# Kernel tuning notes

Hardware: AMD Instinct MI355X
Metric: run time of the kernel (lower is better)

Reference implementation:

```python
import jax, jax.numpy as jnp
import numpy as np

BUFFER_SIZE = 64  # chunk size == sliding window size


def setup_inputs() -> dict:
    key = jax.random.key(0)
    k1, k2, k3, k4 = jax.random.split(key, 4)
    B, S, dim = 4, 8192, 256
    D = dim * 2
    states = jax.random.normal(k1, (B, S, dim, 2), dtype=jnp.float32)
    # projection weights (module inits them to identity; use scaled random for a
    # non-trivial but numerically tame reference)
    Wq = jax.random.normal(k2, (D, D), dtype=jnp.float32) * 0.05
    Wk = jax.random.normal(k3, (D, D), dtype=jnp.float32) * 0.05
    Wv = jax.random.normal(k4, (D, D), dtype=jnp.float32) * 0.05
    return {"states": states, "Wq": Wq, "Wk": Wk, "Wv": Wv}


def reference(states, Wq, Wk, Wv):
    B, S, dim, _ = states.shape
    D = dim * 2
    C = BUFFER_SIZE
    assert S % C == 0 and S > 2 * C
    n = S // C  # number of chunks

    x = states.reshape(B, S, D)
    q = x @ Wq.T
    k = x @ Wk.T
    v = x @ Wv.T

    # chunk: [B, n, C, D]
    qc = q.reshape(B, n, C, D)
    kc = k.reshape(B, n, C, D)
    vc = v.reshape(B, n, C, D)

    # context for chunk i = chunk i-1 ++ chunk i  -> [B, n, 2C, D]
    zeros_blk = jnp.zeros_like(kc[:, :1])
    k_ctx = jnp.concatenate([jnp.concatenate([zeros_blk, kc[:, :-1]], axis=1), kc], axis=2)
    v_ctx = jnp.concatenate([jnp.concatenate([zeros_blk, vc[:, :-1]], axis=1), vc], axis=2)

    scale = 1.0 / jnp.sqrt(jnp.asarray(D, dtype=q.dtype))
    scores = jnp.einsum('bnqd,bnkd->bnqk', qc, k_ctx) * scale  # [B, n, C, 2C]

    # mask: query at local pos qi attends keys strictly before it (global),
    # i.e. context index j < C + qi; chunk 0 has no previous chunk (j >= C).
    qi = jnp.arange(C)[:, None]            # [C,1]
    j = jnp.arange(2 * C)[None, :]         # [1,2C]
    chunk_idx = jnp.arange(n)[:, None, None]
    mask = (j < C + qi)[None] & ((chunk_idx > 0) | (j >= C)[None])  # [n, C, 2C]

    scores = jnp.where(mask[None], scores, jnp.asarray(-1e30, scores.dtype))
    p = jax.nn.softmax(scores, axis=-1)
    # fully-masked rows (only global position 0) -> zero output
    row_valid = jnp.any(mask, axis=-1, keepdims=True)[None].astype(p.dtype)
    p = p * row_valid

    out = jnp.einsum('bnqk,bnkd->bnqd', p, v_ctx).reshape(B, S, D)
    out = out.at[:, 0, :].set(0.0)  # matches retrieved_flat[:, 0, :] = 0.0
    return out.reshape(B, S, dim, 2)
```

## Files before the change

kernel.cpp:

```cpp
#include <hip/hip_runtime.h>

#define SCALE 0.044194173824159216f

typedef _Float16 half8 __attribute__((ext_vector_type(8)));
typedef _Float16 half4 __attribute__((ext_vector_type(4)));
typedef float    f32x4 __attribute__((ext_vector_type(4)));

#define MFMA(A, B, Cc) __builtin_amdgcn_mfma_f32_16x16x32_f16((A), (B), (Cc), 0, 0, 0)

#define X16_OFF 0ull
#define Y16_OFF 33554432ull
#define MT_OFF  67108864ull
#define MP_OFF  68157440ull
#define VT_OFF  100663296ull
#define W16_OFF 134217728ull
#define WS_NEED 135790592ull

typedef __attribute__((address_space(1))) const unsigned int glb_t;
typedef __attribute__((address_space(3))) unsigned int lds_t;

__device__ __forceinline__ void gl16(const void* g, void* l) {
  __builtin_amdgcn_global_load_lds((glb_t*)g, (lds_t*)l, 16, 0, 0);
}

__device__ __forceinline__ half8 ldf64(const _Float16* buf, int row, int colh) {
  int byte = row * 128 + (((colh) << 1) ^ ((row & 7) << 4));
  return *(const half8*)((const char*)buf + byte);
}
__device__ __forceinline__ half8 ldf128(const _Float16* buf, int row, int colh) {
  int byte = row * 256 + (((colh) << 1) ^ ((row & 7) << 4));
  return *(const half8*)((const char*)buf + byte);
}

__global__ __launch_bounds__(256)
void k0_cvt(const float* __restrict__ x, const float* __restrict__ Wq,
            const float* __restrict__ Wk, const float* __restrict__ Wv,
            _Float16* __restrict__ x16, _Float16* __restrict__ w16)
{
  const long long NX = 16777216LL;
  long long base = ((long long)blockIdx.x * 256 + threadIdx.x) * 8;
  const float* src;
  _Float16* dst;
  float sc = 1.0f;
  if (base < NX) {
    src = x + base; dst = x16 + base;
  } else {
    long long o = base - NX;
    int ws = (int)(o >> 18);
    long long oo = o & 262143LL;
    src = (ws == 0 ? Wq : (ws == 1 ? Wk : Wv)) + oo;
    dst = w16 + o;
    if (ws == 0) sc = SCALE;
  }
  const float4* p = (const float4*)src;
  float4 f0 = p[0], f1 = p[1];
  half8 v;
  v[0] = (_Float16)(f0.x * sc); v[1] = (_Float16)(f0.y * sc);
  v[2] = (_Float16)(f0.z * sc); v[3] = (_Float16)(f0.w * sc);
  v[4] = (_Float16)(f1.x * sc); v[5] = (_Float16)(f1.y * sc);
  v[6] = (_Float16)(f1.z * sc); v[7] = (_Float16)(f1.w * sc);
  *(half8*)dst = v;
}

__global__ __launch_bounds__(256)
void kmmA(const float* __restrict__ Wq, const float* __restrict__ Wk,
          float* __restrict__ part)
{
  const int blk = blockIdx.x, t = threadIdx.x;
  const int fc = blk & 7, ot = blk >> 3;
  const int G0 = (ot >> 3) * 16, E0 = (ot & 7) * 64;
  const int gb = G0 + (t & 3) * 4;
  const int e  = E0 + (t >> 2);
  float a0 = 0.f, a1 = 0.f, a2 = 0.f, a3 = 0.f;
  const int f0 = fc * 64;
  #pragma unroll 8
  for (int f = f0; f < f0 + 64; ++f) {
    float4 kv = *(const float4*)(Wk + (size_t)f * 512 + gb);
    float  qv = Wq[(size_t)f * 512 + e];
    a0 += kv.x * qv; a1 += kv.y * qv; a2 += kv.z * qv; a3 += kv.w * qv;
  }
  float* pp = part + (size_t)fc * 262144;
  pp[(size_t)(gb + 0) * 512 + e] = a0;
  pp[(size_t)(gb + 1) * 512 + e] = a1;
  pp[(size_t)(gb + 2) * 512 + e] = a2;
  pp[(size_t)(gb + 3) * 512 + e] = a3;
}

__global__ __launch_bounds__(256)
void kmmB(const float* __restrict__ part, _Float16* __restrict__ Mt)
{
  const int idx = blockIdx.x * 256 + threadIdx.x;
  float s = 0.f;
  #pragma unroll
  for (int fc = 0; fc < 8; ++fc)
    s += part[(size_t)fc * 262144 + idx];
  Mt[idx] = (_Float16)(s * SCALE);
}

__global__ __launch_bounds__(256)
void k1_gemm(const _Float16* __restrict__ x16, const _Float16* __restrict__ w16,
             const _Float16* __restrict__ Mt, _Float16* __restrict__ y16,
             _Float16* __restrict__ vT)
{
  __shared__ _Float16 xs[2][8192];
  __shared__ _Float16 wl[2][8192];

  const int id  = blockIdx.x;
  const int swz = (id & 7) * 256 + (id >> 3);
  const int ntile = swz & 7;
  const int stile = swz >> 3;
  const bool vpath = (ntile >= 4);
  const int tid = threadIdx.x, lane = tid & 63, w = tid >> 6;
  const int l15 = lane & 15, h = lane >> 4;
  const int wm = w >> 1, wn = w & 1;

  const _Float16* xb = x16 + (size_t)stile * 128 * 512;
  const _Float16* wb = vpath ? w16 + (size_t)(1024 + (ntile & 3) * 128) * 512
                             : Mt  + (size_t)((ntile & 3) * 128) * 512;

  int rowi[4], coli[4];
  #pragma unroll
  for (int i = 0; i < 4; ++i) {
    int unit = i * 256 + w * 64 + lane;
    int row = unit >> 3, u = unit & 7;
    rowi[i] = row;
    coli[i] = (u ^ (row & 7)) << 3;
  }

  f32x4 acc[4][4] = {};

  #pragma unroll
  for (int i = 0; i < 4; ++i) {
    int ub = i * 256 + w * 64;
    gl16(xb + (size_t)rowi[i] * 512 + coli[i], &xs[0][ub * 8]);
    gl16(wb + (size_t)rowi[i] * 512 + coli[i], &wl[0][ub * 8]);
  }

  for (int kk = 0; kk < 8; ++kk) {
    const int cur = kk & 1;
    if (kk < 7) {
      const int nxt = cur ^ 1;
      #pragma unroll
      for (int i = 0; i < 4; ++i) {
        int ub = i * 256 + w * 64;
        gl16(xb + (size_t)rowi[i] * 512 + (kk + 1) * 64 + coli[i], &xs[nxt][ub * 8]);
        gl16(wb + (size_t)rowi[i] * 512 + (kk + 1) * 64 + coli[i], &wl[nxt][ub * 8]);
      }
      asm volatile("s_waitcnt vmcnt(8)" ::: "memory");
    } else {
      asm volatile("s_waitcnt vmcnt(0)" ::: "memory");
    }
    __builtin_amdgcn_s_barrier();
    __builtin_amdgcn_sched_barrier(0);

    #pragma unroll
    for (int ks = 0; ks < 2; ++ks) {
      half8 a[4], bf[4];
      if (!vpath) {
        #pragma unroll
        for (int mr = 0; mr < 4; ++mr) a[mr]  = ldf64(xs[cur], wm * 64 + mr * 16 + l15, ks * 32 + h * 8);
        #pragma unroll
        for (int nr = 0; nr < 4; ++nr) bf[nr] = ldf64(wl[cur], wn * 64 + nr * 16 + l15, ks * 32 + h * 8);
      } else {
        #pragma unroll
        for (int mr = 0; mr < 4; ++mr) a[mr]  = ldf64(wl[cur], wm * 64 + mr * 16 + l15, ks * 32 + h * 8);
        #pragma unroll
        for (int nr = 0; nr < 4; ++nr) bf[nr] = ldf64(xs[cur], wn * 64 + nr * 16 + l15, ks * 32 + h * 8);
      }
      #pragma unroll
      for (int mr = 0; mr < 4; ++mr)
        #pragma unroll
        for (int nr = 0; nr < 4; ++nr)
          acc[mr][nr] = MFMA(a[mr], bf[nr], acc[mr][nr]);
    }

    __builtin_amdgcn_sched_barrier(0);
    __builtin_amdgcn_s_barrier();
  }

  if (!vpath) {
    const int m0 = stile * 128 + wm * 64;
    const int n0 = (ntile & 3) * 128 + wn * 64;
    #pragma unroll
    for (int mr = 0; mr < 4; ++mr)
      #pragma unroll
      for (int nr = 0; nr < 4; ++nr)
        #pragma unroll
        for (int r = 0; r < 4; ++r)
          y16[(size_t)(m0 + mr * 16 + h * 4 + r) * 512 + n0 + nr * 16 + l15] =
              (_Float16)acc[mr][nr][r];
  } else {
    const int d0 = (ntile & 3) * 128 + wm * 64;
    const int sg = stile * 128 + wn * 64;
    const int bb = sg >> 13, s0 = sg & 8191;
    _Float16* dst = vT + (size_t)bb * 512 * 8192;
    #pragma unroll
    for (int mr = 0; mr < 4; ++mr)
      #pragma unroll
      for (int nr = 0; nr < 4; ++nr)
        #pragma unroll
        for (int r = 0; r < 4; ++r)
          dst[(size_t)(d0 + mr * 16 + h * 4 + r) * 8192 + s0 + nr * 16 + l15] =
              (_Float16)acc[mr][nr][r];
  }
}

__global__ __launch_bounds__(256)
void k2_attn(const _Float16* __restrict__ y16, const _Float16* __restrict__ x16,
             const _Float16* __restrict__ vT, float* __restrict__ out)
{
  __shared__ _Float16 kj[2][128 * 64];
  __shared__ _Float16 p_lds[64 * 128];

  const int id = blockIdx.x;
  const int sz = (id & 7) * 64 + (id >> 3);
  const int b = sz >> 7, c = sz & 127;
  const int tid = threadIdx.x, lane = tid & 63, w = tid >> 6;
  const int l15 = lane & 15, h = lane >> 4;
  const int jbase = c * 64 - 64;

  const _Float16* qrow = y16 + (size_t)(b * 8192 + c * 64 + w * 16 + l15) * 512;
  half8 qa[16];
  #pragma unroll
  for (int ks = 0; ks < 16; ++ks) qa[ks] = *(const half8*)(qrow + ks * 32 + h * 8);

  const _Float16* kb = x16 + (size_t)b * 8192 * 512;

  f32x4 S[8] = {};
  {
    #pragma unroll
    for (int i = 0; i < 4; ++i) {
      int unit = i * 256 + w * 64 + lane;
      int row = unit >> 3, u = unit & 7;
      int sj = jbase + row; if (sj < 0) sj = 0;
      gl16(kb + (size_t)sj * 512 + ((u ^ (row & 7)) << 3), &kj[0][(i * 256 + w * 64) * 8]);
    }
    int cur = 0;
    for (int ee = 0; ee < 8; ++ee) {
      __syncthreads();
      if (ee < 7) {
        #pragma unroll
        for (int i = 0; i < 4; ++i) {
          int unit = i * 256 + w * 64 + lane;
          int row = unit >> 3, u = unit & 7;
          int sj = jbase + row; if (sj < 0) sj = 0;
          gl16(kb + (size_t)sj * 512 + (ee + 1) * 64 + ((u ^ (row & 7)) << 3),
               &kj[cur ^ 1][(i * 256 + w * 64) * 8]);
        }
      }
      #pragma unroll
      for (int ks = 0; ks < 2; ++ks) {
        #pragma unroll
        for (int nt = 0; nt < 8; ++nt) {
          half8 bf = ldf64(kj[cur], nt * 16 + l15, ks * 32 + h * 8);
          S[nt] = MFMA(qa[ee * 2 + ks], bf, S[nt]);
        }
      }
      cur ^= 1;
    }
  }

  #pragma unroll
  for (int jt = 0; jt < 8; ++jt) {
    int j = jt * 16 + l15;
    #pragma unroll
    for (int r = 0; r < 4; ++r) {
      int ql = w * 16 + h * 4 + r;
      bool valid = (j < 64 + ql) && ((c > 0) || (j >= 64));
      S[jt][r] = valid ? S[jt][r] : -1e30f;
    }
  }
  #pragma unroll
  for (int r = 0; r < 4; ++r) {
    float mx = -1e30f;
    #pragma unroll
    for (int jt = 0; jt < 8; ++jt) mx = fmaxf(mx, S[jt][r]);
    mx = fmaxf(mx, __shfl_xor(mx, 1));
    mx = fmaxf(mx, __shfl_xor(mx, 2));
    mx = fmaxf(mx, __shfl_xor(mx, 4));
    mx = fmaxf(mx, __shfl_xor(mx, 8));
    float sum = 0.f;
    #pragma unroll
    for (int jt = 0; jt < 8; ++jt) {
      float sv = S[jt][r];
      float pe = (sv > -1e29f) ? __expf(sv - mx) : 0.f;
      S[jt][r] = pe;
      sum += pe;
    }
    sum += __shfl_xor(sum, 1);
    sum += __shfl_xor(sum, 2);
    sum += __shfl_xor(sum, 4);
    sum += __shfl_xor(sum, 8);
    float inv = (sum > 0.f) ? (1.0f / sum) : 0.f;
    #pragma unroll
    for (int jt = 0; jt < 8; ++jt) {
      int row = w * 16 + h * 4 + r, col = jt * 16 + l15;
      _Float16 ph = (_Float16)(S[jt][r] * inv);
      *(_Float16*)((char*)p_lds + row * 256 + ((col << 1) ^ ((row & 7) << 4))) = ph;
    }
  }
  half8 pa[4];
  #pragma unroll
  for (int ks = 0; ks < 4; ++ks) {
    int row = w * 16 + l15, colh = ks * 32 + h * 8;
    pa[ks] = *(const half8*)((const char*)p_lds + row * 256 + ((colh << 1) ^ ((row & 7) << 4)));
  }

  const _Float16* vb = vT + (size_t)b * 512 * 8192;
  float* ob = out + (size_t)(b * 8192 + c * 64 + w * 16) * 512;

  __syncthreads();
  #pragma unroll
  for (int i = 0; i < 4; ++i) {
    int unit = i * 256 + w * 64 + lane;
    int row = unit >> 4, u = unit & 15;
    int u2 = (u & 8) | ((u & 7) ^ (row & 7));
    int js = jbase + u2 * 8; if (js < 0) js = 0;
    gl16(vb + (size_t)row * 8192 + js, &kj[0][(i * 256 + w * 64) * 8]);
  }
  int cur = 0;
  for (int dd = 0; dd < 8; ++dd) {
    __syncthreads();
    if (dd < 7) {
      #pragma unroll
      for (int i = 0; i < 4; ++i) {
        int unit = i * 256 + w * 64 + lane;
        int row = unit >> 4, u = unit & 15;
        int u2 = (u & 8) | ((u & 7) ^ (row & 7));
        int js = jbase + u2 * 8; if (js < 0) js = 0;
        gl16(vb + (size_t)((dd + 1) * 64 + row) * 8192 + js, &kj[cur ^ 1][(i * 256 + w * 64) * 8]);
      }
    }
    f32x4 o[4] = {};
    #pragma unroll
    for (int ks = 0; ks < 4; ++ks) {
      #pragma unroll
      for (int nr = 0; nr < 4; ++nr) {
        half8 bf = ldf128(kj[cur], nr * 16 + l15, ks * 32 + h * 8);
        o[nr] = MFMA(pa[ks], bf, o[nr]);
      }
    }
    #pragma unroll
    for (int nr = 0; nr < 4; ++nr)
      #pragma unroll
      for (int r = 0; r < 4; ++r)
        ob[(size_t)(h * 4 + r) * 512 + dd * 64 + nr * 16 + l15] = o[nr][r];
    cur ^= 1;
  }
}

__device__ __forceinline__ int swzb(int row, int colByte) {
  return colByte ^ ((row & 7) << 4);
}
__device__ __forceinline__ half8 ldw_frag(const float* __restrict__ W, int row, int e0) {
  const float4* p = reinterpret_cast<const float4*>(W + ((size_t)row << 9) + e0);
  float4 f0 = p[0];
  float4 f1 = p[1];
  half8 v;
  v[0] = (_Float16)f0.x; v[1] = (_Float16)f0.y; v[2] = (_Float16)f0.z; v[3] = (_Float16)f0.w;
  v[4] = (_Float16)f1.x; v[5] = (_Float16)f1.y; v[6] = (_Float16)f1.z; v[7] = (_Float16)f1.w;
  return v;
}
__device__ __forceinline__ half8 ldl_frag(const unsigned short* buf, int row, int col, int strideBytes) {
  int byte = row * strideBytes + swzb(row, col << 1);
  return *reinterpret_cast<const half8*>(reinterpret_cast<const char*>(buf) + byte);
}

__global__ __launch_bounds__(256, 1)
void ep_fused(const float* __restrict__ x, const float* __restrict__ Wq,
              const float* __restrict__ Wk, const float* __restrict__ Wv,
              float* __restrict__ out)
{
  __shared__ unsigned short xs[128 * 512];
  __shared__ unsigned short kv[64 * 128];
  __shared__ unsigned short pq[64 * 128];

  const int bc   = blockIdx.x;
  const int b    = bc >> 7;
  const int c    = bc & 127;
  const int tid  = threadIdx.x;
  const int lane = tid & 63;
  const int w    = tid >> 6;
  const int l15  = lane & 15;
  const int h    = lane >> 4;

  const float* xb = x + (size_t)b * (8192 * 512);
  #pragma unroll
  for (int i = 0; i < 32; ++i) {
    int unit = tid + (i << 8);
    int row  = unit >> 6;
    int e0   = (unit & 63) << 3;
    half8 v;
    if (c == 0 && row < 64) {
      #pragma unroll
      for (int t = 0; t < 8; ++t) v[t] = (_Float16)0.0f;
    } else {
      int s = c * 64 - 64 + row;
      const float4* p = reinterpret_cast<const float4*>(xb + (size_t)s * 512 + e0);
      float4 f0 = p[0], f1 = p[1];
      v[0] = (_Float16)f0.x; v[1] = (_Float16)f0.y; v[2] = (_Float16)f0.z; v[3] = (_Float16)f0.w;
      v[4] = (_Float16)f1.x; v[5] = (_Float16)f1.y; v[6] = (_Float16)f1.z; v[7] = (_Float16)f1.w;
    }
    int byte = (row << 10) + swzb(row, e0 << 1);
    *reinterpret_cast<half8*>(reinterpret_cast<char*>(xs) + byte) = v;
  }
  __syncthreads();

  f32x4 Sacc[8] = {};
  const int d0 = (w << 4) + (h << 2);

  for (int dt = 0; dt < 8; ++dt) {
    const int drow = (dt << 6) + (w << 4) + l15;

    f32x4 qa[4] = {};
    for (int ks = 0; ks < 16; ++ks) {
      half8 a = ldw_frag(Wq, drow, (ks << 5) + (h << 3));
      #pragma unroll
      for (int nt = 0; nt < 4; ++nt) {
        half8 bf = ldl_frag(xs, 64 + (nt << 4) + l15, (ks << 5) + (h << 3), 1024);
        qa[nt] = MFMA(a, bf, qa[nt]);
      }
    }
    #pragma unroll
    for (int nt = 0; nt < 4; ++nt) {
      int q = (nt << 4) + l15;
      half4 hv;
      hv[0] = (_Float16)qa[nt][0]; hv[1] = (_Float16)qa[nt][1];
      hv[2] = (_Float16)qa[nt][2]; hv[3] = (_Float16)qa[nt][3];
      *reinterpret_cast<half4*>(reinterpret_cast<char*>(pq) + q * 128 + swzb(q, d0 << 1)) = hv;
    }

    f32x4 ka[8] = {};
    for (int ks = 0; ks < 16; ++ks) {
      half8 a = ldw_frag(Wk, drow, (ks << 5) + (h << 3));
      #pragma unroll
      for (int nt = 0; nt < 8; ++nt) {
        half8 bf = ldl_frag(xs, (nt << 4) + l15, (ks << 5) + (h << 3), 1024);
        ka[nt] = MFMA(a, bf, ka[nt]);
      }
    }
    #pragma unroll
    for (int nt = 0; nt < 8; ++nt) {
      int j = (nt << 4) + l15;
      half4 hv;
      hv[0] = (_Float16)ka[nt][0]; hv[1] = (_Float16)ka[nt][1];
      hv[2] = (_Float16)ka[nt][2]; hv[3] = (_Float16)ka[nt][3];
      *reinterpret_cast<half4*>(reinterpret_cast<char*>(kv) + j * 128 + swzb(j, d0 << 1)) = hv;
    }
    __syncthreads();

    #pragma unroll
    for (int ksd = 0; ksd < 2; ++ksd) {
      half8 a = ldl_frag(pq, (w << 4) + l15, (ksd << 5) + (h << 3), 128);
      #pragma unroll
      for (int nt = 0; nt < 8; ++nt) {
        half8 bf = ldl_frag(kv, (nt << 4) + l15, (ksd << 5) + (h << 3), 128);
        Sacc[nt] = MFMA(a, bf, Sacc[nt]);
      }
    }
    __syncthreads();
  }

  const float scale = SCALE;
  #pragma unroll
  for (int nt = 0; nt < 8; ++nt) {
    int j = (nt << 4) + l15;
    #pragma unroll
    for (int r = 0; r < 4; ++r) {
      int qrow = (w << 4) + (h << 2) + r;
      bool valid = (j < 64 + qrow) && ((c > 0) || (j >= 64));
      Sacc[nt][r] = valid ? Sacc[nt][r] * scale : -1e30f;
    }
  }
  float inv[4];
  #pragma unroll
  for (int r = 0; r < 4; ++r) {
    float mx = -1e30f;
    #pragma unroll
    for (int nt = 0; nt < 8; ++nt) mx = fmaxf(mx, Sacc[nt][r]);
    mx = fmaxf(mx, __shfl_xor(mx, 1));
    mx = fmaxf(mx, __shfl_xor(mx, 2));
    mx = fmaxf(mx, __shfl_xor(mx, 4));
    mx = fmaxf(mx, __shfl_xor(mx, 8));
    float sum = 0.f;
    #pragma unroll
    for (int nt = 0; nt < 8; ++nt) {
      float sv = Sacc[nt][r];
      float pe = (sv > -1e29f) ? __expf(sv - mx) : 0.f;
      Sacc[nt][r] = pe;
      sum += pe;
    }
    sum += __shfl_xor(sum, 1);
    sum += __shfl_xor(sum, 2);
    sum += __shfl_xor(sum, 4);
    sum += __shfl_xor(sum, 8);
    inv[r] = (sum > 0.f) ? (1.0f / sum) : 0.f;
  }
  #pragma unroll
  for (int nt = 0; nt < 8; ++nt) {
    int j = (nt << 4) + l15;
    #pragma unroll
    for (int r = 0; r < 4; ++r) {
      int qrow = (w << 4) + (h << 2) + r;
      _Float16 ph = (_Float16)(Sacc[nt][r] * inv[r]);
      *reinterpret_cast<_Float16*>(reinterpret_cast<char*>(pq) + qrow * 256 + swzb(qrow, j << 1)) = ph;
    }
  }
  __syncthreads();

  for (int dt = 0; dt < 8; ++dt) {
    const int dcol = (dt << 6) + (w << 4) + l15;

    f32x4 va[8] = {};
    for (int ks = 0; ks < 16; ++ks) {
      half8 bf = ldw_frag(Wv, dcol, (ks << 5) + (h << 3));
      #pragma unroll
      for (int mt = 0; mt < 8; ++mt) {
        half8 a = ldl_frag(xs, (mt << 4) + l15, (ks << 5) + (h << 3), 1024);
        va[mt] = MFMA(a, bf, va[mt]);
      }
    }
    {
      int dl = (w << 4) + l15;
      #pragma unroll
      for (int mt = 0; mt < 8; ++mt) {
        int j0 = (mt << 4) + (h << 2);
        half4 hv;
        hv[0] = (_Float16)va[mt][0]; hv[1] = (_Float16)va[mt][1];
        hv[2] = (_Float16)va[mt][2]; hv[3] = (_Float16)va[mt][3];
        *reinterpret_cast<half4*>(reinterpret_cast<char*>(kv) + dl * 256 + swzb(dl, j0 << 1)) = hv;
      }
    }
    __syncthreads();

    f32x4 oa[4] = {};
    #pragma unroll
    for (int ks = 0; ks < 4; ++ks) {
      half8 a = ldl_frag(pq, (w << 4) + l15, (ks << 5) + (h << 3), 256);
      #pragma unroll
      for (int nt = 0; nt < 4; ++nt) {
        half8 bf = ldl_frag(kv, (nt << 4) + l15, (ks << 5) + (h << 3), 256);
        oa[nt] = MFMA(a, bf, oa[nt]);
      }
    }
    #pragma unroll
    for (int nt = 0; nt < 4; ++nt) {
      int d = (dt << 6) + (nt << 4) + l15;
      #pragma unroll
      for (int r = 0; r < 4; ++r) {
        int qrow = (w << 4) + (h << 2) + r;
        out[((size_t)(b * 8192 + (c << 6) + qrow) << 9) + d] = oa[nt][r];
      }
    }
    __syncthreads();
  }
}

extern "C" void kernel_launch(void* const* d_in, const int* in_sizes, int n_in,
                              void* d_out, int out_size, void* d_ws, size_t ws_size,
                              hipStream_t stream) {
  const float* x  = (const float*)d_in[0];
  const float* Wq = (const float*)d_in[1];
  const float* Wk = (const float*)d_in[2];
  const float* Wv = (const float*)d_in[3];
  float* out = (float*)d_out;
  (void)in_sizes; (void)n_in; (void)out_size;

  if (d_ws != nullptr && ws_size >= WS_NEED) {
    char* ws = (char*)d_ws;
    _Float16* x16 = (_Float16*)(ws + X16_OFF);
    _Float16* y16 = (_Float16*)(ws + Y16_OFF);
    _Float16* Mt  = (_Float16*)(ws + MT_OFF);
    float*    Mp  = (float*)(ws + MP_OFF);
    _Float16* vT  = (_Float16*)(ws + VT_OFF);
    _Float16* w16 = (_Float16*)(ws + W16_OFF);

    hipLaunchKernelGGL(kmmA, dim3(2048), dim3(256), 0, stream, Wq, Wk, Mp);
    hipLaunchKernelGGL(k0_cvt, dim3(8576), dim3(256), 0, stream, x, Wq, Wk, Wv, x16, w16);
    hipLaunchKernelGGL(kmmB, dim3(1024), dim3(256), 0, stream, Mp, Mt);
    hipLaunchKernelGGL(k1_gemm, dim3(2048), dim3(256), 0, stream, x16, w16, Mt, y16, vT);
    hipLaunchKernelGGL(k2_attn, dim3(512), dim3(256), 0, stream, y16, x16, vT, out);
  } else {
    hipLaunchKernelGGL(ep_fused, dim3(512), dim3(256), 0, stream, x, Wq, Wk, Wv, out);
  }
}
```

Baseline: 117.9 us.

## Merge conversion and Wq·Wk kernels; pipeline attention loads with explicit waitcnt

The fp16 conversion kernel and the Wk^T·Wq partial-product kernel become one launch that selects its role by block index, removing one launch and letting the two jobs share the GPU. In the attention kernel, load addresses are precomputed and both loops are fully unrolled. __syncthreads is replaced by explicit vmcnt waits plus s_barrier and sched_barrier so the next tile's global-to-LDS load stays in flight during the MFMAs. The first V tile is also prefetched before the softmax stage. This relies on careful manual vmcnt accounting, and the merged kernel's two block types have uneven work.

Result: faster. 114.6 us (-2.8%).

```diff
diff --git a/kernel.cpp b/kernel.cpp
--- a/kernel.cpp
+++ b/kernel.cpp
@@ -33,57 +33,55 @@
 }
 
 __global__ __launch_bounds__(256)
-void k0_cvt(const float* __restrict__ x, const float* __restrict__ Wq,
-            const float* __restrict__ Wk, const float* __restrict__ Wv,
-            _Float16* __restrict__ x16, _Float16* __restrict__ w16)
+void k0m(const float* __restrict__ x, const float* __restrict__ Wq,
+         const float* __restrict__ Wk, const float* __restrict__ Wv,
+         _Float16* __restrict__ x16, _Float16* __restrict__ w16,
+         float* __restrict__ part)
 {
-  const long long NX = 16777216LL;
-  long long base = ((long long)blockIdx.x * 256 + threadIdx.x) * 8;
-  const float* src;
-  _Float16* dst;
-  float sc = 1.0f;
-  if (base < NX) {
-    src = x + base; dst = x16 + base;
+  if (blockIdx.x < 8576) {
+    const long long NX = 16777216LL;
+    long long base = ((long long)blockIdx.x * 256 + threadIdx.x) * 8;
+    const float* src;
+    _Float16* dst;
+    float sc = 1.0f;
+    if (base < NX) {
+      src = x + base; dst = x16 + base;
+    } else {
+      long long o = base - NX;
+      int ws = (int)(o >> 18);
+      long long oo = o & 262143LL;
+      src = (ws == 0 ? Wq : (ws == 1 ? Wk : Wv)) + oo;
+      dst = w16 + o;
+      if (ws == 0) sc = SCALE;
+    }
+    const float4* p = (const float4*)src;
+    float4 f0 = p[0], f1 = p[1];
+    half8 v;
+    v[0] = (_Float16)(f0.x * sc); v[1] = (_Float16)(f0.y * sc);
+    v[2] = (_Float16)(f0.z * sc); v[3] = (_Float16)(f0.w * sc);
+    v[4] = (_Float16)(f1.x * sc); v[5] = (_Float16)(f1.y * sc);
+    v[6] = (_Float16)(f1.z * sc); v[7] = (_Float16)(f1.w * sc);
+    *(half8*)dst = v;
   } else {
-    long long o = base - NX;
-    int ws = (int)(o >> 18);
-    long long oo = o & 262143LL;
-    src = (ws == 0 ? Wq : (ws == 1 ? Wk : Wv)) + oo;
-    dst = w16 + o;
-    if (ws == 0) sc = SCALE;
-  }
-  const float4* p = (const float4*)src;
-  float4 f0 = p[0], f1 = p[1];
-  half8 v;
-  v[0] = (_Float16)(f0.x * sc); v[1] = (_Float16)(f0.y * sc);
-  v[2] = (_Float16)(f0.z * sc); v[3] = (_Float16)(f0.w * sc);
-  v[4] = (_Float16)(f1.x * sc); v[5] = (_Float16)(f1.y * sc);
-  v[6] = (_Float16)(f1.z * sc); v[7] = (_Float16)(f1.w * sc);
-  *(half8*)dst = v;
-}
-
-__global__ __launch_bounds__(256)
-void kmmA(const float* __restrict__ Wq, const float* __restrict__ Wk,
-          float* __restrict__ part)
-{
-  const int blk = blockIdx.x, t = threadIdx.x;
-  const int fc = blk & 7, ot = blk >> 3;
-  const int G0 = (ot >> 3) * 16, E0 = (ot & 7) * 64;
-  const int gb = G0 + (t & 3) * 4;
-  const int e  = E0 + (t >> 2);
-  float a0 = 0.f, a1 = 0.f, a2 = 0.f, a3 = 0.f;
-  const int f0 = fc * 64;
-  #pragma unroll 8
-  for (int f = f0; f < f0 + 64; ++f) {
-    float4 kv = *(const float4*)(Wk + (size_t)f * 512 + gb);
-    float  qv = Wq[(size_t)f * 512 + e];
-    a0 += kv.x * qv; a1 += kv.y * qv; a2 += kv.z * qv; a3 += kv.w * qv;
-  }
-  float* pp = part + (size_t)fc * 262144;
-  pp[(size_t)(gb + 0) * 512 + e] = a0;
-  pp[(size_t)(gb + 1) * 512 + e] = a1;
-  pp[(size_t)(gb + 2) * 512 + e] = a2;
-  pp[(size_t)(gb + 3) * 512 + e] = a3;
+    const int blk = blockIdx.x - 8576, t = threadIdx.x;
+    const int fc = blk & 7, ot = blk >> 3;
+    const int G0 = (ot >> 3) * 16, E0 = (ot & 7) * 64;
+    const int gb = G0 + (t & 3) * 4;
+    const int e  = E0 + (t >> 2);
+    float a0 = 0.f, a1 = 0.f, a2 = 0.f, a3 = 0.f;
+    const int f0 = fc * 64;
+    #pragma unroll 8
+    for (int f = f0; f < f0 + 64; ++f) {
+      float4 kv = *(const float4*)(Wk + (size_t)f * 512 + gb);
+      float  qv = Wq[(size_t)f * 512 + e];
+      a0 += kv.x * qv; a1 += kv.y * qv; a2 += kv.z * qv; a3 += kv.w * qv;
+    }
+    float* pp = part + (size_t)fc * 262144;
+    pp[(size_t)(gb + 0) * 512 + e] = a0;
+    pp[(size_t)(gb + 1) * 512 + e] = a1;
+    pp[(size_t)(gb + 2) * 512 + e] = a2;
+    pp[(size_t)(gb + 3) * 512 + e] = a3;
+  }
 }
 
 __global__ __launch_bounds__(256)
@@ -225,40 +223,62 @@
   for (int ks = 0; ks < 16; ++ks) qa[ks] = *(const half8*)(qrow + ks * 32 + h * 8);
 
   const _Float16* kb = x16 + (size_t)b * 8192 * 512;
+  const _Float16* vb = vT + (size_t)b * 512 * 8192;
+
+  int srow[4], scol[4];
+  #pragma unroll
+  for (int i = 0; i < 4; ++i) {
+    int unit = i * 256 + w * 64 + lane;
+    int row = unit >> 3, u = unit & 7;
+    int sj = jbase + row; if (sj < 0) sj = 0;
+    srow[i] = sj;
+    scol[i] = (u ^ (row & 7)) << 3;
+  }
+  int prow[4], pjs[4];
+  #pragma unroll
+  for (int i = 0; i < 4; ++i) {
+    int unit = i * 256 + w * 64 + lane;
+    int row = unit >> 4, u = unit & 15;
+    int u2 = (u & 8) | ((u & 7) ^ (row & 7));
+    int js = jbase + u2 * 8; if (js < 0) js = 0;
+    prow[i] = row;
+    pjs[i] = js;
+  }
 
   f32x4 S[8] = {};
-  {
-    #pragma unroll
-    for (int i = 0; i < 4; ++i) {
-      int unit = i * 256 + w * 64 + lane;
-      int row = unit >> 3, u = unit & 7;
-      int sj = jbase + row; if (sj < 0) sj = 0;
-      gl16(kb + (size_t)sj * 512 + ((u ^ (row & 7)) << 3), &kj[0][(i * 256 + w * 64) * 8]);
-    }
-    int cur = 0;
-    for (int ee = 0; ee < 8; ++ee) {
-      __syncthreads();
-      if (ee < 7) {
-        #pragma unroll
-        for (int i = 0; i < 4; ++i) {
-          int unit = i * 256 + w * 64 + lane;
-          int row = unit >> 3, u = unit & 7;
-          int sj = jbase + row; if (sj < 0) sj = 0;
-          gl16(kb + (size_t)sj * 512 + (ee + 1) * 64 + ((u ^ (row & 7)) << 3),
-               &kj[cur ^ 1][(i * 256 + w * 64) * 8]);
-        }
-      }
-      #pragma unroll
-      for (int ks = 0; ks < 2; ++ks) {
-        #pragma unroll
-        for (int nt = 0; nt < 8; ++nt) {
-          half8 bf = ldf64(kj[cur], nt * 16 + l15, ks * 32 + h * 8);
-          S[nt] = MFMA(qa[ee * 2 + ks], bf, S[nt]);
-        }
-      }
-      cur ^= 1;
-    }
-  }
+  #pragma unroll
+  for (int i = 0; i < 4; ++i)
+    gl16(kb + (size_t)srow[i] * 512 + scol[i], &kj[0][(i * 256 + w * 64) * 8]);
+
+  #pragma unroll
+  for (int ee = 0; ee < 8; ++ee) {
+    if (ee < 7) {
+      #pragma unroll
+      for (int i = 0; i < 4; ++i)
+        gl16(kb + (size_t)srow[i] * 512 + (ee + 1) * 64 + scol[i],
+             &kj[(ee + 1) & 1][(i * 256 + w * 64) * 8]);
+      asm volatile("s_waitcnt vmcnt(4)" ::: "memory");
+    } else {
+      asm volatile("s_waitcnt vmcnt(0)" ::: "memory");
+    }
+    __builtin_amdgcn_s_barrier();
+    __builtin_amdgcn_sched_barrier(0);
+
+    #pragma unroll
+    for (int ks = 0; ks < 2; ++ks) {
+      #pragma unroll
+      for (int nt = 0; nt < 8; ++nt) {
+        half8 bf = ldf64(kj[ee & 1], nt * 16 + l15, ks * 32 + h * 8);
+        S[nt] = MFMA(qa[ee * 2 + ks], bf, S[nt]);
+      }
+    }
+    __builtin_amdgcn_sched_barrier(0);
+    __builtin_amdgcn_s_barrier();
+  }
+
+  #pragma unroll
+  for (int i = 0; i < 4; ++i)
+    gl16(vb + (size_t)prow[i] * 8192 + pjs[i], &kj[0][(i * 256 + w * 64) * 8]);
 
   #pragma unroll
   for (int jt = 0; jt < 8; ++jt) {
@@ -306,37 +326,27 @@
     pa[ks] = *(const half8*)((const char*)p_lds + row * 256 + ((colh << 1) ^ ((row & 7) << 4)));
   }
 
-  const _Float16* vb = vT + (size_t)b * 512 * 8192;
   float* ob = out + (size_t)(b * 8192 + c * 64 + w * 16) * 512;
-
-  __syncthreads();
-  #pragma unroll
-  for (int i = 0; i < 4; ++i) {
-    int unit = i * 256 + w * 64 + lane;
-    int row = unit >> 4, u = unit & 15;
-    int u2 = (u & 8) | ((u & 7) ^ (row & 7));
-    int js = jbase + u2 * 8; if (js < 0) js = 0;
-    gl16(vb + (size_t)row * 8192 + js, &kj[0][(i * 256 + w * 64) * 8]);
-  }
-  int cur = 0;
+  #pragma unroll
   for (int dd = 0; dd < 8; ++dd) {
-    __syncthreads();
     if (dd < 7) {
       #pragma unroll
-      for (int i = 0; i < 4; ++i) {
-        int unit = i * 256 + w * 64 + lane;
-        int row = unit >> 4, u = unit & 15;
-        int u2 = (u & 8) | ((u & 7) ^ (row & 7));
-        int js = jbase + u2 * 8; if (js < 0) js = 0;
-        gl16(vb + (size_t)((dd + 1) * 64 + row) * 8192 + js, &kj[cur ^ 1][(i * 256 + w * 64) * 8]);
-      }
-    }
+      for (int i = 0; i < 4; ++i)
+        gl16(vb + (size_t)((dd + 1) * 64 + prow[i]) * 8192 + pjs[i],
+             &kj[(dd + 1) & 1][(i * 256 + w * 64) * 8]);
+      asm volatile("s_waitcnt vmcnt(4)" ::: "memory");
+    } else {
+      asm volatile("s_waitcnt vmcnt(0)" ::: "memory");
+    }
+    __builtin_amdgcn_s_barrier();
+    __builtin_amdgcn_sched_barrier(0);
+
     f32x4 o[4] = {};
     #pragma unroll
     for (int ks = 0; ks < 4; ++ks) {
       #pragma unroll
       for (int nr = 0; nr < 4; ++nr) {
-        half8 bf = ldf128(kj[cur], nr * 16 + l15, ks * 32 + h * 8);
+        half8 bf = ldf128(kj[dd & 1], nr * 16 + l15, ks * 32 + h * 8);
         o[nr] = MFMA(pa[ks], bf, o[nr]);
       }
     }
@@ -345,7 +355,8 @@
       #pragma unroll
       for (int r = 0; r < 4; ++r)
         ob[(size_t)(h * 4 + r) * 512 + dd * 64 + nr * 16 + l15] = o[nr][r];
-    cur ^= 1;
+    __builtin_amdgcn_sched_barrier(0);
+    __builtin_amdgcn_s_barrier();
   }
 }
 
@@ -575,8 +586,7 @@
     _Float16* vT  = (_Float16*)(ws + VT_OFF);
     _Float16* w16 = (_Float16*)(ws + W16_OFF);
 
-    hipLaunchKernelGGL(kmmA, dim3(2048), dim3(256), 0, stream, Wq, Wk, Mp);
-    hipLaunchKernelGGL(k0_cvt, dim3(8576), dim3(256), 0, stream, x, Wq, Wk, Wv, x16, w16);
+    hipLaunchKernelGGL(k0m, dim3(10624), dim3(256), 0, stream, x, Wq, Wk, Wv, x16, w16, Mp);
     hipLaunchKernelGGL(kmmB, dim3(1024), dim3(256), 0, stream, Mp, Mt);
     hipLaunchKernelGGL(k1_gemm, dim3(2048), dim3(256), 0, stream, x16, w16, Mt, y16, vT);
     hipLaunchKernelGGL(k2_attn, dim3(512), dim3(256), 0, stream, y16, x16, vT, out);
```
